# Performance work log

Hardware: AMD Instinct MI355X
Metric: run time of the kernel (lower is better)

Reference implementation:

```python
import jax, jax.numpy as jnp
import numpy as np
from functools import partial

EPS = 1e-5
SCALE = 2
NUM_BLOCKS = 2


def _layernorm(x, g, b):
    mu = jnp.mean(x, axis=-1, keepdims=True)
    var = jnp.var(x, axis=-1, keepdims=True)
    return (x - mu) * jax.lax.rsqrt(var + EPS) * g + b


def _rwkv(tokens, td, Wk, Wv, Wr, Wo, ln_g, ln_b):
    # tokens: (B, N, C)
    x = _layernorm(tokens, ln_g, ln_b)
    k = jnp.einsum('bnc,oc->bno', x, Wk)
    v = jnp.einsum('bnc,oc->bno', x, Wv)
    r = jax.nn.sigmoid(jnp.einsum('bnc,oc->bno', x, Wr))
    decay = jnp.exp(-jax.nn.relu(td))  # (C,)

    def step(state, inp):
        kt, vt, rt = inp  # each (B, C)
        state = state * decay + kt
        return state, rt * (state + vt)

    B, N, C = tokens.shape
    init = jnp.zeros((B, C), dtype=tokens.dtype)
    # scan over token axis
    _, yT = jax.lax.scan(step, init, (k.transpose(1, 0, 2), v.transpose(1, 0, 2), r.transpose(1, 0, 2)))
    y = yT.transpose(1, 0, 2)  # (B, N, C)
    return jnp.einsum('bnc,oc->bno', y, Wo)


def reference(x, global_state, cond_gw, cond_gb, cond_bw, cond_bb,
              td, Wk, Wv, Wr, Wo, ln_g, ln_b, gp_w, gp_b, bp_w, bp_b):
    B, C, H, W = x.shape
    Hp, Wp = H * SCALE, W * SCALE
    # bilinear upsample, half-pixel centers == torch align_corners=False
    x_up = jax.image.resize(x, (B, C, Hp, Wp), method='bilinear')
    tokens = x_up.reshape(B, C, Hp * Wp).transpose(0, 2, 1)  # (B, N, C)
    # semantic conditioning (FiLM from global state)
    gamma = (global_state @ cond_gw.T + cond_gb)[:, None, :]
    beta = (global_state @ cond_bw.T + cond_bb)[:, None, :]
    tokens = tokens * (1.0 + gamma) + beta

    out = x_up
    cur = tokens
    for i in range(NUM_BLOCKS):
        if i > 0:
            cur = out.reshape(B, C, Hp * Wp).transpose(0, 2, 1)
        t = _rwkv(cur, td[i], Wk[i], Wv[i], Wr[i], Wo[i], ln_g[i], ln_b[i])
        g = jnp.einsum('bnc,oc->bno', t, gp_w[i]) + gp_b[i]
        bt = jnp.einsum('bnc,oc->bno', t, bp_w[i]) + bp_b[i]
        g = g.transpose(0, 2, 1).reshape(B, C, Hp, Wp)
        bt = bt.transpose(0, 2, 1).reshape(B, C, Hp, Wp)
        out = out * (1.0 + jnp.tanh(g)) + bt
    return out


def setup_inputs() -> dict:
    key = jax.random.key(0)
    ks = jax.random.split(key, 16)
    B, C, H, W = 8, 128, 64, 64
    w_scale = 0.02
    inp = {
        'x': jax.random.normal(ks[0], (B, C, H, W), jnp.float32),
        'global_state': jax.random.normal(ks[1], (B, C), jnp.float32),
        'cond_gw': jax.random.normal(ks[2], (C, C), jnp.float32) * w_scale,
        'cond_gb': jnp.zeros((C,), jnp.float32),
        'cond_bw': jax.random.normal(ks[3], (C, C), jnp.float32) * w_scale,
        'cond_bb': jnp.zeros((C,), jnp.float32),
        'td': jax.random.uniform(ks[4], (NUM_BLOCKS, C), jnp.float32),
        'Wk': jax.random.normal(ks[5], (NUM_BLOCKS, C, C), jnp.float32) * w_scale,
        'Wv': jax.random.normal(ks[6], (NUM_BLOCKS, C, C), jnp.float32) * w_scale,
        'Wr': jax.random.normal(ks[7], (NUM_BLOCKS, C, C), jnp.float32) * w_scale,
        'Wo': jax.random.normal(ks[8], (NUM_BLOCKS, C, C), jnp.float32) * w_scale,
        'ln_g': jnp.ones((NUM_BLOCKS, C), jnp.float32),
        'ln_b': jnp.zeros((NUM_BLOCKS, C), jnp.float32),
        'gp_w': jax.random.normal(ks[9], (NUM_BLOCKS, C, C), jnp.float32) * w_scale,
        'gp_b': jnp.zeros((NUM_BLOCKS, C), jnp.float32),
        'bp_w': jax.random.normal(ks[10], (NUM_BLOCKS, C, C), jnp.float32) * w_scale,
        'bp_b': jnp.zeros((NUM_BLOCKS, C), jnp.float32),
    }
    return inp
```

## Files before the change

kernel.cpp:

```cpp
#include <hip/hip_runtime.h>
#include <hip/hip_bf16.h>

#define BB 8
#define CC 128
#define NN 16384
#define MM (BB * NN)
#define NCH 128
#define CLN 128

typedef __attribute__((ext_vector_type(8))) short short8;
typedef __attribute__((ext_vector_type(4))) float floatx4;
typedef unsigned short u16;
typedef unsigned int u32;

__device__ __forceinline__ float bf2f(u16 h) {
  u32 u = ((u32)h) << 16;
  return __builtin_bit_cast(float, u);
}
__device__ __forceinline__ u16 f2bf(float f) {
  u32 u = __builtin_bit_cast(u32, f);
  u32 r = u + 0x7FFFu + ((u >> 16) & 1u);
  return (u16)(r >> 16);
}

__global__ void film_kernel(const float* __restrict__ gs, const float* __restrict__ gw,
                            const float* __restrict__ gb, const float* __restrict__ bw,
                            const float* __restrict__ bb, float* __restrict__ gamma,
                            float* __restrict__ beta) {
  int idx = blockIdx.x * 256 + threadIdx.x;
  int b = idx >> 7, c = idx & 127;
  float sg = 0.f, sb = 0.f;
  for (int j = 0; j < 128; ++j) {
    float g = gs[b * 128 + j];
    sg += g * gw[c * 128 + j];
    sb += g * bw[c * 128 + j];
  }
  gamma[idx] = sg + gb[c];
  beta[idx] = sb + bb[c];
}

__global__ void convert_kernel(const float* __restrict__ Wk, const float* __restrict__ Wv,
                               const float* __restrict__ Wr, const float* __restrict__ Wo,
                               const float* __restrict__ gp, const float* __restrict__ bp,
                               u16* __restrict__ dst) {
  int idx = blockIdx.x * 256 + threadIdx.x;
  int which = idx >> 15;
  int off = idx & 32767;
  const float* s;
  switch (which) {
    case 0: s = Wk; break; case 1: s = Wv; break; case 2: s = Wr; break;
    case 3: s = Wo; break; case 4: s = gp; break; default: s = bp; break;
  }
  dst[idx] = f2bf(s[off]);
}

template <int UPS>
__global__ __launch_bounds__(256) void prep_kernel(
    const float* __restrict__ src, const float* __restrict__ gamma,
    const float* __restrict__ beta, const float* __restrict__ lng,
    const float* __restrict__ lnb, float* __restrict__ outp, u16* __restrict__ xn) {
  __shared__ float tile[64][129];
  __shared__ float smu[64], srs[64];
  int bidx = blockIdx.x;
  int half = bidx & 1;
  int ho = (bidx >> 1) & 127;
  int b = bidx >> 8;
  int wo0 = half * 64;
  int tid = threadIdx.x;
  int tk = tid & 63;
  int wo = wo0 + tk;
  int c0 = tid >> 6;
  int j0 = 0, j1 = 0, i0 = 0, i1 = 0;
  float wy0 = 0.f, wy1 = 0.f, wx0 = 0.f, wx1 = 0.f;
  if (UPS) {
    int jj = ho >> 1;
    if ((ho & 1) == 0) { j0 = jj > 0 ? jj - 1 : 0; j1 = jj; wy0 = 0.25f; wy1 = 0.75f; }
    else               { j0 = jj; j1 = jj < 63 ? jj + 1 : 63; wy0 = 0.75f; wy1 = 0.25f; }
    int ii = wo >> 1;
    if ((wo & 1) == 0) { i0 = ii > 0 ? ii - 1 : 0; i1 = ii; wx0 = 0.25f; wx1 = 0.75f; }
    else               { i0 = ii; i1 = ii < 63 ? ii + 1 : 63; wx0 = 0.75f; wx1 = 0.25f; }
  }
  for (int it = 0; it < 32; ++it) {
    int c = it * 4 + c0;
    float v;
    if (UPS) {
      const float* xp = src + ((size_t)(b * 128 + c)) * 4096;
      v = wy0 * (wx0 * xp[j0 * 64 + i0] + wx1 * xp[j0 * 64 + i1]) +
          wy1 * (wx0 * xp[j1 * 64 + i0] + wx1 * xp[j1 * 64 + i1]);
      outp[((size_t)(b * 128 + c)) * 16384 + ho * 128 + wo] = v;
      v = v * (1.f + gamma[b * 128 + c]) + beta[b * 128 + c];
    } else {
      v = src[((size_t)(b * 128 + c)) * 16384 + ho * 128 + wo];
    }
    tile[tk][c] = v;
  }
  __syncthreads();
  {
    int token = tid >> 2, q = tid & 3;
    float s = 0.f, s2 = 0.f;
    for (int j = 0; j < 32; ++j) { float v = tile[token][q * 32 + j]; s += v; s2 += v * v; }
    s += __shfl_xor(s, 1); s2 += __shfl_xor(s2, 1);
    s += __shfl_xor(s, 2); s2 += __shfl_xor(s2, 2);
    if (q == 0) {
      float mu = s * 0.0078125f;
      float var = s2 * 0.0078125f - mu * mu;
      smu[token] = mu;
      srs[token] = rsqrtf(var + 1e-5f);
    }
  }
  __syncthreads();
  size_t base = ((size_t)b * 16384 + ho * 128 + wo0) * 128;
  for (int it = 0; it < 32; ++it) {
    int idx = it * 256 + tid;
    int token = idx >> 7, c = idx & 127;
    float v = (tile[token][c] - smu[token]) * srs[token] * lng[c] + lnb[c];
    xn[base + idx] = f2bf(v);
  }
}

__global__ __launch_bounds__(256) void gemm_kvr_kernel(
    const u16* __restrict__ A, const u16* __restrict__ W0, const u16* __restrict__ W1,
    const u16* __restrict__ W2, const float* __restrict__ td, u16* __restrict__ outK,
    u16* __restrict__ outV, u16* __restrict__ outR, float* __restrict__ Sbuf) {
  __shared__ u16 Alds[128 * 128];
  __shared__ u16 Wlds[128 * 128];
  __shared__ float Sred[512];
  int tid = threadIdx.x;
  int wave = tid >> 6, lane = tid & 63;
  int l15 = lane & 15, l4 = lane >> 4;
  size_t row0 = (size_t)blockIdx.x * 128;
#pragma unroll
  for (int it = 0; it < 8; ++it) {
    int idx = it * 256 + tid;
    int rr = idx >> 4, s = idx & 15;
    uint4 d = *(const uint4*)(A + (row0 + rr) * 128 + s * 8);
    *(uint4*)(&Alds[rr * 128 + ((s ^ (rr & 15)) << 3)]) = d;
  }
  const u16* Wsarr[3] = {W0, W1, W2};
#pragma unroll
  for (int wsi = 0; wsi < 3; ++wsi) {
#pragma unroll
    for (int it = 0; it < 8; ++it) {
      int idx = it * 256 + tid;
      int rr = idx >> 4, s = idx & 15;
      uint4 d = *(const uint4*)(Wsarr[wsi] + rr * 128 + s * 8);
      *(uint4*)(&Wlds[rr * 128 + ((s ^ (rr & 15)) << 3)]) = d;
    }
    __syncthreads();
    floatx4 acc[2][8];
#pragma unroll
    for (int mi = 0; mi < 2; ++mi)
#pragma unroll
      for (int ni = 0; ni < 8; ++ni) acc[mi][ni] = (floatx4){0.f, 0.f, 0.f, 0.f};
#pragma unroll
    for (int kk = 0; kk < 4; ++kk) {
      int seg = kk * 4 + l4;
      short8 a0 = *(const short8*)(&Alds[(wave * 32 + l15) * 128 + ((seg ^ l15) << 3)]);
      short8 a1 = *(const short8*)(&Alds[(wave * 32 + 16 + l15) * 128 + ((seg ^ l15) << 3)]);
#pragma unroll
      for (int ni = 0; ni < 8; ++ni) {
        short8 bfr = *(const short8*)(&Wlds[(ni * 16 + l15) * 128 + ((seg ^ l15) << 3)]);
        acc[0][ni] = __builtin_amdgcn_mfma_f32_16x16x32_bf16(a0, bfr, acc[0][ni], 0, 0, 0);
        acc[1][ni] = __builtin_amdgcn_mfma_f32_16x16x32_bf16(a1, bfr, acc[1][ni], 0, 0, 0);
      }
    }
#pragma unroll
    for (int mi = 0; mi < 2; ++mi) {
#pragma unroll
      for (int ni = 0; ni < 8; ++ni) {
        int col = ni * 16 + l15;
#pragma unroll
        for (int j = 0; j < 4; ++j) {
          size_t row = row0 + wave * 32 + mi * 16 + l4 * 4 + j;
          float val = acc[mi][ni][j];
          if (wsi == 0) outK[row * 128 + col] = f2bf(val);
          else if (wsi == 1) outV[row * 128 + col] = f2bf(val);
          else outR[row * 128 + col] = f2bf(1.f / (1.f + __expf(-val)));
        }
      }
    }
    if (wsi == 0) {
      int T0 = wave * 32 + l4 * 4;
#pragma unroll
      for (int ni = 0; ni < 8; ++ni) {
        int c = ni * 16 + l15;
        float a = fmaxf(td[c], 0.f);
        float E = __expf(-a * (float)(127 - T0));
        float r1 = __expf(a);
        float r2 = r1 * r1, r4 = r2 * r2, r8 = r4 * r4, r16 = r8 * r8;
        float w = E, sum;
        sum  = w * acc[0][ni][0]; w *= r1;
        sum += w * acc[0][ni][1]; w *= r1;
        sum += w * acc[0][ni][2]; w *= r1;
        sum += w * acc[0][ni][3];
        w = E * r16;
        sum += w * acc[1][ni][0]; w *= r1;
        sum += w * acc[1][ni][1]; w *= r1;
        sum += w * acc[1][ni][2]; w *= r1;
        sum += w * acc[1][ni][3];
        sum += __shfl_xor(sum, 16);
        sum += __shfl_xor(sum, 32);
        if (l4 == 0) Sred[wave * 128 + c] = sum;
      }
    }
    __syncthreads();
    if (wsi == 0 && tid < 128) {
      float s = Sred[tid] + Sred[128 + tid] + Sred[256 + tid] + Sred[384 + tid];
      Sbuf[(blockIdx.x & 127) * 1024 + (blockIdx.x >> 7) * 128 + tid] = s;
    }
  }
}

__global__ __launch_bounds__(256) void scan2_kernel(const float* __restrict__ S,
                                                    const float* __restrict__ td,
                                                    float* __restrict__ init) {
  int wave = threadIdx.x >> 6, lane = threadIdx.x & 63;
  int bc = blockIdx.x * 4 + wave;
  int c = bc & 127;
  float a1 = __expf(-fmaxf(td[c], 0.f) * 128.f);
  float s0 = S[(2 * lane) * 1024 + bc];
  float s1 = S[(2 * lane + 1) * 1024 + bc];
  float s = s1 + a1 * s0;
  float a = a1 * a1;
  for (int off = 1; off < 64; off <<= 1) {
    float ss = __shfl_up(s, off);
    float aa = __shfl_up(a, off);
    if (lane >= off) { s = s + a * ss; a = a * aa; }
  }
  float e = __shfl_up(s, 1);
  if (lane == 0) e = 0.f;
  init[(2 * lane) * 1024 + bc] = e;
  init[(2 * lane + 1) * 1024 + bc] = a1 * e + s0;
}

__global__ __launch_bounds__(512, 4) void tail_kernel(
    const u16* __restrict__ k, const u16* __restrict__ v, const u16* __restrict__ r,
    const float* __restrict__ init, const float* __restrict__ td,
    const u16* __restrict__ Wo, const u16* __restrict__ Wg, const u16* __restrict__ Wb,
    const float* __restrict__ gpb, const float* __restrict__ bpb,
    float* __restrict__ outp) {
  __shared__ u32 SMEM[8192];
  __shared__ float SC[512];
  u16* Y = (u16*)SMEM;
  u16* T2 = (u16*)SMEM;
  u32* MB = SMEM;

  int tid = threadIdx.x;
  int wave = tid >> 6, lane = tid & 63;
  int l15 = lane & 15, l4 = lane >> 4;
  int b = blockIdx.x >> 7;
  int chunk = blockIdx.x & 127;
  size_t ebase = ((size_t)b * 16384 + (size_t)chunk * 128) * 128;

  {
    int c = tid & 127;
    int sub = tid >> 7;
    float a = fmaxf(td[c], 0.f);
    float d = __expf(-a);
    const u16* kp = k + ebase + (size_t)sub * 32 * 128 + c;
    const u16* vp = v + ebase + (size_t)sub * 32 * 128 + c;
    const u16* rp = r + ebase + (size_t)sub * 32 * 128 + c;
    float s = 0.f;
#pragma unroll
    for (int t = 0; t < 32; ++t) s = s * d + bf2f(kp[t * 128]);
    SC[sub * 128 + c] = s;
    __syncthreads();
    float st = init[chunk * 1024 + b * 128 + c];
    float d32 = __expf(-a * 32.f);
    for (int j = 0; j < sub; ++j) st = st * d32 + SC[j * 128 + c];
    int cs = c >> 3, cl = c & 7;
#pragma unroll
    for (int t = 0; t < 32; ++t) {
      int tg = sub * 32 + t;
      st = st * d + bf2f(kp[t * 128]);
      float y = bf2f(rp[t * 128]) * (st + bf2f(vp[t * 128]));
      Y[tg * 128 + (((cs ^ (tg & 15)) << 3) | cl)] = f2bf(y);
    }
  }
  __syncthreads();

  int ob = wave * 16;
  short8 wof[4];
#pragma unroll
  for (int kk = 0; kk < 4; ++kk)
    wof[kk] = *(const short8*)(Wo + (ob + l15) * 128 + kk * 32 + l4 * 8);
  floatx4 acc[8];
#pragma unroll
  for (int ni = 0; ni < 8; ++ni) acc[ni] = (floatx4){0.f, 0.f, 0.f, 0.f};
#pragma unroll
  for (int kk = 0; kk < 4; ++kk) {
    int seg = kk * 4 + l4;
#pragma unroll
    for (int ni = 0; ni < 8; ++ni) {
      short8 yf = *(const short8*)(&Y[(ni * 16 + l15) * 128 + ((seg ^ l15) << 3)]);
      acc[ni] = __builtin_amdgcn_mfma_f32_16x16x32_bf16(wof[kk], yf, acc[ni], 0, 0, 0);
    }
  }
  __syncthreads();

#pragma unroll
  for (int ni = 0; ni < 8; ++ni) {
    int tok = ni * 16 + l15;
#pragma unroll
    for (int j = 0; j < 4; j += 2) {
      int o = ob + l4 * 4 + j;
      u32 pack = (u32)f2bf(acc[ni][j]) | ((u32)f2bf(acc[ni][j + 1]) << 16);
      int pos = tok * 128 + ((((o >> 3) ^ (tok & 15)) << 3) | (o & 7));
      *(u32*)(T2 + pos) = pack;
    }
  }
  __syncthreads();

  short8 wgf[4], wbf2[4];
#pragma unroll
  for (int kk = 0; kk < 4; ++kk) {
    wgf[kk]  = *(const short8*)(Wg + (ob + l15) * 128 + kk * 32 + l4 * 8);
    wbf2[kk] = *(const short8*)(Wb + (ob + l15) * 128 + kk * 32 + l4 * 8);
  }
  floatx4 ag[8], ab[8];
#pragma unroll
  for (int ni = 0; ni < 8; ++ni) {
    ag[ni] = (floatx4){0.f, 0.f, 0.f, 0.f};
    ab[ni] = (floatx4){0.f, 0.f, 0.f, 0.f};
  }
#pragma unroll
  for (int kk = 0; kk < 4; ++kk) {
    int seg = kk * 4 + l4;
#pragma unroll
    for (int ni = 0; ni < 8; ++ni) {
      short8 tf = *(const short8*)(&T2[(ni * 16 + l15) * 128 + ((seg ^ l15) << 3)]);
      ag[ni] = __builtin_amdgcn_mfma_f32_16x16x32_bf16(wgf[kk], tf, ag[ni], 0, 0, 0);
      ab[ni] = __builtin_amdgcn_mfma_f32_16x16x32_bf16(wbf2[kk], tf, ab[ni], 0, 0, 0);
    }
  }
  __syncthreads();

#pragma unroll
  for (int h = 0; h < 2; ++h) {
    if ((wave >> 2) == h) {
      int orel0 = (wave & 3) * 16;
#pragma unroll
      for (int ni = 0; ni < 8; ++ni) {
        int tok = ni * 16 + l15;
#pragma unroll
        for (int j = 0; j < 4; ++j) {
          int orel = orel0 + l4 * 4 + j;
          int o = h * 64 + orel;
          float g = ag[ni][j] + gpb[o];
          float t1 = __expf(2.f * g);
          float m = 2.f - 2.f / (t1 + 1.f);
          float bt = ab[ni][j] + bpb[o];
          int rot = ((orel & 3) << 2) | ((orel >> 2) & 3);
          MB[orel * 128 + ((((tok >> 3) ^ rot) << 3) | (tok & 7))] =
              (u32)f2bf(m) | ((u32)f2bf(bt) << 16);
        }
      }
    }
    __syncthreads();
#pragma unroll
    for (int it = 0; it < 2; ++it) {
      int idx = it * 512 + tid;
      int orel = idx >> 4, seg = idx & 15;
      int o = h * 64 + orel;
      int rot = ((orel & 3) << 2) | ((orel >> 2) & 3);
      int sp = ((seg ^ rot) << 3);
      uint4 mb0 = *(const uint4*)(&MB[orel * 128 + sp]);
      uint4 mb1 = *(const uint4*)(&MB[orel * 128 + sp + 4]);
      float* op = outp + ((size_t)(b * 128 + o)) * 16384 + chunk * 128 + seg * 8;
      float4 o0 = *(float4*)op;
      float4 o1 = *(float4*)(op + 4);
      o0.x = o0.x * bf2f((u16)(mb0.x & 0xffff)) + bf2f((u16)(mb0.x >> 16));
      o0.y = o0.y * bf2f((u16)(mb0.y & 0xffff)) + bf2f((u16)(mb0.y >> 16));
      o0.z = o0.z * bf2f((u16)(mb0.z & 0xffff)) + bf2f((u16)(mb0.z >> 16));
      o0.w = o0.w * bf2f((u16)(mb0.w & 0xffff)) + bf2f((u16)(mb0.w >> 16));
      o1.x = o1.x * bf2f((u16)(mb1.x & 0xffff)) + bf2f((u16)(mb1.x >> 16));
      o1.y = o1.y * bf2f((u16)(mb1.y & 0xffff)) + bf2f((u16)(mb1.y >> 16));
      o1.z = o1.z * bf2f((u16)(mb1.z & 0xffff)) + bf2f((u16)(mb1.z >> 16));
      o1.w = o1.w * bf2f((u16)(mb1.w & 0xffff)) + bf2f((u16)(mb1.w >> 16));
      *(float4*)op = o0;
      *(float4*)(op + 4) = o1;
    }
    __syncthreads();
  }
}

extern "C" void kernel_launch(void* const* d_in, const int* in_sizes, int n_in,
                              void* d_out, int out_size, void* d_ws, size_t ws_size,
                              hipStream_t stream) {
  const float* x        = (const float*)d_in[0];
  const float* gs       = (const float*)d_in[1];
  const float* cond_gw  = (const float*)d_in[2];
  const float* cond_gb  = (const float*)d_in[3];
  const float* cond_bw  = (const float*)d_in[4];
  const float* cond_bb  = (const float*)d_in[5];
  const float* td       = (const float*)d_in[6];
  const float* Wk       = (const float*)d_in[7];
  const float* Wv       = (const float*)d_in[8];
  const float* Wr       = (const float*)d_in[9];
  const float* Wo       = (const float*)d_in[10];
  const float* ln_g     = (const float*)d_in[11];
  const float* ln_b     = (const float*)d_in[12];
  const float* gp_w     = (const float*)d_in[13];
  const float* gp_b     = (const float*)d_in[14];
  const float* bp_w     = (const float*)d_in[15];
  const float* bp_b     = (const float*)d_in[16];
  float* outp = (float*)d_out;

  char* w = (char*)d_ws;
  float* gamma = (float*)w; w += 4096;
  float* beta  = (float*)w; w += 4096;
  u16* wbf     = (u16*)w;   w += 6 * 2 * 16384 * sizeof(u16);
  u16* xn      = (u16*)w;   w += (size_t)MM * 128 * sizeof(u16);
  u16* kbuf    = (u16*)w;   w += (size_t)MM * 128 * sizeof(u16);
  u16* vbuf    = (u16*)w;   w += (size_t)MM * 128 * sizeof(u16);
  u16* rbuf    = (u16*)w;   w += (size_t)MM * 128 * sizeof(u16);
  float* Sbuf  = (float*)w; w += NCH * 1024 * sizeof(float);
  float* ibuf  = (float*)w; w += NCH * 1024 * sizeof(float);

  film_kernel<<<4, 256, 0, stream>>>(gs, cond_gw, cond_gb, cond_bw, cond_bb, gamma, beta);
  convert_kernel<<<768, 256, 0, stream>>>(Wk, Wv, Wr, Wo, gp_w, bp_w, wbf);

  for (int blk = 0; blk < 2; ++blk) {
    const u16* bWk = wbf + 0 * 32768 + blk * 16384;
    const u16* bWv = wbf + 1 * 32768 + blk * 16384;
    const u16* bWr = wbf + 2 * 32768 + blk * 16384;
    const u16* bWo = wbf + 3 * 32768 + blk * 16384;
    const u16* bGp = wbf + 4 * 32768 + blk * 16384;
    const u16* bBp = wbf + 5 * 32768 + blk * 16384;
    const float* tdi = td + blk * 128;

    if (blk == 0)
      prep_kernel<1><<<2048, 256, 0, stream>>>(x, gamma, beta, ln_g, ln_b, outp, xn);
    else
      prep_kernel<0><<<2048, 256, 0, stream>>>(outp, nullptr, nullptr, ln_g + 128,
                                               ln_b + 128, nullptr, xn);

    gemm_kvr_kernel<<<1024, 256, 0, stream>>>(xn, bWk, bWv, bWr, tdi,
                                              kbuf, vbuf, rbuf, Sbuf);
    scan2_kernel<<<256, 256, 0, stream>>>(Sbuf, tdi, ibuf);
    tail_kernel<<<1024, 512, 0, stream>>>(kbuf, vbuf, rbuf, ibuf, tdi,
                                          bWo, bGp, bBp, gp_b + blk * 128,
                                          bp_b + blk * 128, outp);
  }
}
```

Before: 265.7 us.

## Fuse intra-chunk scan into KVR GEMM, emit partial y and decayed r

The GEMM kernel now runs the within-chunk linear recurrence in registers, using cross-lane shuffles and shared memory to carry state between waves. It writes a partial output y (computed with zero initial state) and a decay-weighted r, so two bf16 intermediates are stored instead of three k/v/r buffers. The tail kernel then only applies the chunk's incoming state as y + rd*init, with vectorized loads, replacing its serial per-token scan. This reduces global memory traffic and serial work, but adds register pressure (several accumulator sets are live, with launch bounds of 2 blocks) and takes a small precision risk from storing r·decay in bf16.

New measurement: 268.9 us. No clear change (+1.2%).

```diff
diff --git a/kernel.cpp b/kernel.cpp
--- a/kernel.cpp
+++ b/kernel.cpp
@@ -118,17 +118,18 @@
   }
 }
 
-__global__ __launch_bounds__(256) void gemm_kvr_kernel(
-    const u16* __restrict__ A, const u16* __restrict__ W0, const u16* __restrict__ W1,
-    const u16* __restrict__ W2, const float* __restrict__ td, u16* __restrict__ outK,
-    u16* __restrict__ outV, u16* __restrict__ outR, float* __restrict__ Sbuf) {
+__global__ __launch_bounds__(256, 2) void gemm_y_kernel(
+    const u16* __restrict__ A, const u16* __restrict__ Wv_, const u16* __restrict__ Wr_,
+    const u16* __restrict__ Wk_, const float* __restrict__ td,
+    u16* __restrict__ outY, u16* __restrict__ outRD, float* __restrict__ Sbuf) {
   __shared__ u16 Alds[128 * 128];
   __shared__ u16 Wlds[128 * 128];
-  __shared__ float Sred[512];
+  __shared__ float SWT[512];
   int tid = threadIdx.x;
   int wave = tid >> 6, lane = tid & 63;
   int l15 = lane & 15, l4 = lane >> 4;
   size_t row0 = (size_t)blockIdx.x * 128;
+
 #pragma unroll
   for (int it = 0; it < 8; ++it) {
     int idx = it * 256 + tid;
@@ -136,78 +137,192 @@
     uint4 d = *(const uint4*)(A + (row0 + rr) * 128 + s * 8);
     *(uint4*)(&Alds[rr * 128 + ((s ^ (rr & 15)) << 3)]) = d;
   }
-  const u16* Wsarr[3] = {W0, W1, W2};
-#pragma unroll
-  for (int wsi = 0; wsi < 3; ++wsi) {
-#pragma unroll
-    for (int it = 0; it < 8; ++it) {
-      int idx = it * 256 + tid;
-      int rr = idx >> 4, s = idx & 15;
-      uint4 d = *(const uint4*)(Wsarr[wsi] + rr * 128 + s * 8);
-      *(uint4*)(&Wlds[rr * 128 + ((s ^ (rr & 15)) << 3)]) = d;
-    }
-    __syncthreads();
-    floatx4 acc[2][8];
-#pragma unroll
-    for (int mi = 0; mi < 2; ++mi)
-#pragma unroll
-      for (int ni = 0; ni < 8; ++ni) acc[mi][ni] = (floatx4){0.f, 0.f, 0.f, 0.f};
-#pragma unroll
-    for (int kk = 0; kk < 4; ++kk) {
-      int seg = kk * 4 + l4;
-      short8 a0 = *(const short8*)(&Alds[(wave * 32 + l15) * 128 + ((seg ^ l15) << 3)]);
-      short8 a1 = *(const short8*)(&Alds[(wave * 32 + 16 + l15) * 128 + ((seg ^ l15) << 3)]);
-#pragma unroll
-      for (int ni = 0; ni < 8; ++ni) {
-        short8 bfr = *(const short8*)(&Wlds[(ni * 16 + l15) * 128 + ((seg ^ l15) << 3)]);
-        acc[0][ni] = __builtin_amdgcn_mfma_f32_16x16x32_bf16(a0, bfr, acc[0][ni], 0, 0, 0);
-        acc[1][ni] = __builtin_amdgcn_mfma_f32_16x16x32_bf16(a1, bfr, acc[1][ni], 0, 0, 0);
+#pragma unroll
+  for (int it = 0; it < 8; ++it) {
+    int idx = it * 256 + tid;
+    int rr = idx >> 4, s = idx & 15;
+    uint4 d = *(const uint4*)(Wv_ + rr * 128 + s * 8);
+    *(uint4*)(&Wlds[rr * 128 + ((s ^ (rr & 15)) << 3)]) = d;
+  }
+  float av[8], dd[8], d4a[8];
+#pragma unroll
+  for (int ni = 0; ni < 8; ++ni) {
+    float a = fmaxf(td[ni * 16 + l15], 0.f);
+    av[ni] = a;
+    float d = __expf(-a);
+    dd[ni] = d;
+    float d2 = d * d;
+    d4a[ni] = d2 * d2;
+  }
+  __syncthreads();
+
+  floatx4 accv[2][8];
+#pragma unroll
+  for (int mi = 0; mi < 2; ++mi)
+#pragma unroll
+    for (int ni = 0; ni < 8; ++ni) accv[mi][ni] = (floatx4){0.f, 0.f, 0.f, 0.f};
+#pragma unroll
+  for (int kk = 0; kk < 4; ++kk) {
+    int seg = kk * 4 + l4;
+    short8 a0 = *(const short8*)(&Alds[(wave * 32 + l15) * 128 + ((seg ^ l15) << 3)]);
+    short8 a1 = *(const short8*)(&Alds[(wave * 32 + 16 + l15) * 128 + ((seg ^ l15) << 3)]);
+#pragma unroll
+    for (int ni = 0; ni < 8; ++ni) {
+      short8 bfr = *(const short8*)(&Wlds[(ni * 16 + l15) * 128 + ((seg ^ l15) << 3)]);
+      accv[0][ni] = __builtin_amdgcn_mfma_f32_16x16x32_bf16(a0, bfr, accv[0][ni], 0, 0, 0);
+      accv[1][ni] = __builtin_amdgcn_mfma_f32_16x16x32_bf16(a1, bfr, accv[1][ni], 0, 0, 0);
+    }
+  }
+  __syncthreads();
+#pragma unroll
+  for (int it = 0; it < 8; ++it) {
+    int idx = it * 256 + tid;
+    int rr = idx >> 4, s = idx & 15;
+    uint4 d = *(const uint4*)(Wr_ + rr * 128 + s * 8);
+    *(uint4*)(&Wlds[rr * 128 + ((s ^ (rr & 15)) << 3)]) = d;
+  }
+  __syncthreads();
+  floatx4 accr[2][8];
+#pragma unroll
+  for (int mi = 0; mi < 2; ++mi)
+#pragma unroll
+    for (int ni = 0; ni < 8; ++ni) accr[mi][ni] = (floatx4){0.f, 0.f, 0.f, 0.f};
+#pragma unroll
+  for (int kk = 0; kk < 4; ++kk) {
+    int seg = kk * 4 + l4;
+    short8 a0 = *(const short8*)(&Alds[(wave * 32 + l15) * 128 + ((seg ^ l15) << 3)]);
+    short8 a1 = *(const short8*)(&Alds[(wave * 32 + 16 + l15) * 128 + ((seg ^ l15) << 3)]);
+#pragma unroll
+    for (int ni = 0; ni < 8; ++ni) {
+      short8 bfr = *(const short8*)(&Wlds[(ni * 16 + l15) * 128 + ((seg ^ l15) << 3)]);
+      accr[0][ni] = __builtin_amdgcn_mfma_f32_16x16x32_bf16(a0, bfr, accr[0][ni], 0, 0, 0);
+      accr[1][ni] = __builtin_amdgcn_mfma_f32_16x16x32_bf16(a1, bfr, accr[1][ni], 0, 0, 0);
+    }
+  }
+  u32 rvp[2][8][2], rp[2][8][2];
+#pragma unroll
+  for (int mi = 0; mi < 2; ++mi) {
+#pragma unroll
+    for (int ni = 0; ni < 8; ++ni) {
+      int c = ni * 16 + l15;
+      int T0 = wave * 32 + mi * 16 + l4 * 4;
+      float w = __expf(-av[ni] * (float)(T0 + 1));
+      float rs[4], rv[4];
+#pragma unroll
+      for (int j = 0; j < 4; ++j) {
+        float sg = 1.f / (1.f + __expf(-accr[mi][ni][j]));
+        rs[j] = sg;
+        rv[j] = sg * accv[mi][ni][j];
+        outRD[(row0 + T0 + j) * 128 + c] = f2bf(sg * w);
+        w *= dd[ni];
       }
-    }
+      rvp[mi][ni][0] = (u32)f2bf(rv[0]) | ((u32)f2bf(rv[1]) << 16);
+      rvp[mi][ni][1] = (u32)f2bf(rv[2]) | ((u32)f2bf(rv[3]) << 16);
+      rp[mi][ni][0] = (u32)f2bf(rs[0]) | ((u32)f2bf(rs[1]) << 16);
+      rp[mi][ni][1] = (u32)f2bf(rs[2]) | ((u32)f2bf(rs[3]) << 16);
+    }
+  }
+  __syncthreads();
+#pragma unroll
+  for (int it = 0; it < 8; ++it) {
+    int idx = it * 256 + tid;
+    int rr = idx >> 4, s = idx & 15;
+    uint4 d = *(const uint4*)(Wk_ + rr * 128 + s * 8);
+    *(uint4*)(&Wlds[rr * 128 + ((s ^ (rr & 15)) << 3)]) = d;
+  }
+  __syncthreads();
+  floatx4 acck[2][8];
+#pragma unroll
+  for (int mi = 0; mi < 2; ++mi)
+#pragma unroll
+    for (int ni = 0; ni < 8; ++ni) acck[mi][ni] = (floatx4){0.f, 0.f, 0.f, 0.f};
+#pragma unroll
+  for (int kk = 0; kk < 4; ++kk) {
+    int seg = kk * 4 + l4;
+    short8 a0 = *(const short8*)(&Alds[(wave * 32 + l15) * 128 + ((seg ^ l15) << 3)]);
+    short8 a1 = *(const short8*)(&Alds[(wave * 32 + 16 + l15) * 128 + ((seg ^ l15) << 3)]);
+#pragma unroll
+    for (int ni = 0; ni < 8; ++ni) {
+      short8 bfr = *(const short8*)(&Wlds[(ni * 16 + l15) * 128 + ((seg ^ l15) << 3)]);
+      acck[0][ni] = __builtin_amdgcn_mfma_f32_16x16x32_bf16(a0, bfr, acck[0][ni], 0, 0, 0);
+      acck[1][ni] = __builtin_amdgcn_mfma_f32_16x16x32_bf16(a1, bfr, acck[1][ni], 0, 0, 0);
+    }
+  }
+  float Elr[2][8];
+  float B0r[8];
+#pragma unroll
+  for (int ni = 0; ni < 8; ++ni) {
+    float d = dd[ni], d4 = d4a[ni];
+    float d8 = d4 * d4, d16 = d8 * d8;
+    float I[2];
 #pragma unroll
     for (int mi = 0; mi < 2; ++mi) {
-#pragma unroll
-      for (int ni = 0; ni < 8; ++ni) {
-        int col = ni * 16 + l15;
-#pragma unroll
-        for (int j = 0; j < 4; ++j) {
-          size_t row = row0 + wave * 32 + mi * 16 + l4 * 4 + j;
-          float val = acc[mi][ni][j];
-          if (wsi == 0) outK[row * 128 + col] = f2bf(val);
-          else if (wsi == 1) outV[row * 128 + col] = f2bf(val);
-          else outR[row * 128 + col] = f2bf(1.f / (1.f + __expf(-val)));
-        }
+      float p0 = acck[mi][ni][0];
+      float p1 = d * p0 + acck[mi][ni][1];
+      float p2 = d * p1 + acck[mi][ni][2];
+      float p3 = d * p2 + acck[mi][ni][3];
+      acck[mi][ni][0] = p0; acck[mi][ni][1] = p1;
+      acck[mi][ni][2] = p2; acck[mi][ni][3] = p3;
+      float Iv = p3;
+      float t1 = __shfl_up(Iv, 16);
+      if (l4 >= 1) Iv += d4 * t1;
+      float t2 = __shfl_up(Iv, 32);
+      if (l4 >= 2) Iv += d8 * t2;
+      float ex = __shfl_up(Iv, 16);
+      Elr[mi][ni] = (l4 == 0) ? 0.f : ex;
+      I[mi] = Iv;
+    }
+    float B0 = __shfl(I[0], 48 + l15);
+    float B1 = __shfl(I[1], 48 + l15);
+    B0r[ni] = B0;
+    if (l4 == 0) SWT[wave * 128 + ni * 16 + l15] = B1 + d16 * B0;
+  }
+  __syncthreads();
+  u16* YW = Wlds;
+#pragma unroll
+  for (int ni = 0; ni < 8; ++ni) {
+    int c = ni * 16 + l15;
+    float d = dd[ni], d4 = d4a[ni];
+    float d8 = d4 * d4, d12 = d8 * d4, d16 = d8 * d8, d32 = d16 * d16;
+    float e = 0.f;
+#pragma unroll
+    for (int wv = 0; wv < 3; ++wv)
+      if (wv < wave) e = e * d32 + SWT[wv * 128 + c];
+    float d4l = (l4 == 0) ? 1.f : ((l4 == 1) ? d4 : ((l4 == 2) ? d8 : d12));
+#pragma unroll
+    for (int mi = 0; mi < 2; ++mi) {
+      float Emi = (mi == 0) ? e : (e * d16 + B0r[ni]);
+      float Sb = Elr[mi][ni] + d4l * Emi;
+      float w = d;
+#pragma unroll
+      for (int j = 0; j < 4; ++j) {
+        float s = acck[mi][ni][j] + w * Sb;
+        w *= d;
+        float rvv = bf2f((u16)(rvp[mi][ni][j >> 1] >> ((j & 1) * 16)));
+        float rss = bf2f((u16)(rp[mi][ni][j >> 1] >> ((j & 1) * 16)));
+        float y = rvv + rss * s;
+        int row = wave * 32 + mi * 16 + l4 * 4 + j;
+        int colsw = c ^ (((row >> 2) & 3) << 4);
+        YW[row * 128 + colsw] = f2bf(y);
       }
     }
-    if (wsi == 0) {
-      int T0 = wave * 32 + l4 * 4;
-#pragma unroll
-      for (int ni = 0; ni < 8; ++ni) {
-        int c = ni * 16 + l15;
-        float a = fmaxf(td[c], 0.f);
-        float E = __expf(-a * (float)(127 - T0));
-        float r1 = __expf(a);
-        float r2 = r1 * r1, r4 = r2 * r2, r8 = r4 * r4, r16 = r8 * r8;
-        float w = E, sum;
-        sum  = w * acc[0][ni][0]; w *= r1;
-        sum += w * acc[0][ni][1]; w *= r1;
-        sum += w * acc[0][ni][2]; w *= r1;
-        sum += w * acc[0][ni][3];
-        w = E * r16;
-        sum += w * acc[1][ni][0]; w *= r1;
-        sum += w * acc[1][ni][1]; w *= r1;
-        sum += w * acc[1][ni][2]; w *= r1;
-        sum += w * acc[1][ni][3];
-        sum += __shfl_xor(sum, 16);
-        sum += __shfl_xor(sum, 32);
-        if (l4 == 0) Sred[wave * 128 + c] = sum;
-      }
-    }
-    __syncthreads();
-    if (wsi == 0 && tid < 128) {
-      float s = Sred[tid] + Sred[128 + tid] + Sred[256 + tid] + Sred[384 + tid];
-      Sbuf[(blockIdx.x & 127) * 1024 + (blockIdx.x >> 7) * 128 + tid] = s;
-    }
+  }
+  if (tid < 128) {
+    float a = fmaxf(td[tid], 0.f);
+    float d32 = __expf(-32.f * a);
+    float e = 0.f;
+#pragma unroll
+    for (int wv = 0; wv < 4; ++wv) e = e * d32 + SWT[wv * 128 + tid];
+    Sbuf[(blockIdx.x & 127) * 1024 + (blockIdx.x >> 7) * 128 + tid] = e;
+  }
+  __syncthreads();
+#pragma unroll
+  for (int it = 0; it < 8; ++it) {
+    int idx = it * 256 + tid;
+    int row = idx >> 4, cb = (idx & 15) * 8;
+    int csw = cb ^ (((row >> 2) & 3) << 4);
+    uint4 dv = *(const uint4*)(&YW[row * 128 + csw]);
+    *(uint4*)(outY + (row0 + row) * 128 + cb) = dv;
   }
 }
 
@@ -234,13 +349,13 @@
 }
 
 __global__ __launch_bounds__(512, 4) void tail_kernel(
-    const u16* __restrict__ k, const u16* __restrict__ v, const u16* __restrict__ r,
-    const float* __restrict__ init, const float* __restrict__ td,
+    const u16* __restrict__ yl, const u16* __restrict__ rd,
+    const float* __restrict__ init,
     const u16* __restrict__ Wo, const u16* __restrict__ Wg, const u16* __restrict__ Wb,
     const float* __restrict__ gpb, const float* __restrict__ bpb,
     float* __restrict__ outp) {
   __shared__ u32 SMEM[8192];
-  __shared__ float SC[512];
+  __shared__ float IL[128];
   u16* Y = (u16*)SMEM;
   u16* T2 = (u16*)SMEM;
   u32* MB = SMEM;
@@ -252,30 +367,27 @@
   int chunk = blockIdx.x & 127;
   size_t ebase = ((size_t)b * 16384 + (size_t)chunk * 128) * 128;
 
-  {
-    int c = tid & 127;
-    int sub = tid >> 7;
-    float a = fmaxf(td[c], 0.f);
-    float d = __expf(-a);
-    const u16* kp = k + ebase + (size_t)sub * 32 * 128 + c;
-    const u16* vp = v + ebase + (size_t)sub * 32 * 128 + c;
-    const u16* rp = r + ebase + (size_t)sub * 32 * 128 + c;
-    float s = 0.f;
-#pragma unroll
-    for (int t = 0; t < 32; ++t) s = s * d + bf2f(kp[t * 128]);
-    SC[sub * 128 + c] = s;
-    __syncthreads();
-    float st = init[chunk * 1024 + b * 128 + c];
-    float d32 = __expf(-a * 32.f);
-    for (int j = 0; j < sub; ++j) st = st * d32 + SC[j * 128 + c];
-    int cs = c >> 3, cl = c & 7;
-#pragma unroll
-    for (int t = 0; t < 32; ++t) {
-      int tg = sub * 32 + t;
-      st = st * d + bf2f(kp[t * 128]);
-      float y = bf2f(rp[t * 128]) * (st + bf2f(vp[t * 128]));
-      Y[tg * 128 + (((cs ^ (tg & 15)) << 3) | cl)] = f2bf(y);
-    }
+  if (tid < 128) IL[tid] = init[chunk * 1024 + b * 128 + tid];
+  __syncthreads();
+
+#pragma unroll
+  for (int it = 0; it < 4; ++it) {
+    int idx = it * 512 + tid;
+    int t = idx >> 4;
+    int c8 = (idx & 15) * 8;
+    uint4 yv = *(const uint4*)(yl + ebase + (size_t)t * 128 + c8);
+    uint4 rv = *(const uint4*)(rd + ebase + (size_t)t * 128 + c8);
+    u32 o[4];
+    u32 yq[4] = {yv.x, yv.y, yv.z, yv.w};
+    u32 rq[4] = {rv.x, rv.y, rv.z, rv.w};
+#pragma unroll
+    for (int q = 0; q < 4; ++q) {
+      float y0 = bf2f((u16)(yq[q] & 0xffff)) + bf2f((u16)(rq[q] & 0xffff)) * IL[c8 + 2 * q];
+      float y1 = bf2f((u16)(yq[q] >> 16)) + bf2f((u16)(rq[q] >> 16)) * IL[c8 + 2 * q + 1];
+      o[q] = (u32)f2bf(y0) | ((u32)f2bf(y1) << 16);
+    }
+    uint4 ov = {o[0], o[1], o[2], o[3]};
+    *(uint4*)(&Y[t * 128 + (((c8 >> 3) ^ (t & 15)) << 3)]) = ov;
   }
   __syncthreads();
 
@@ -411,9 +523,8 @@
   float* beta  = (float*)w; w += 4096;
   u16* wbf     = (u16*)w;   w += 6 * 2 * 16384 * sizeof(u16);
   u16* xn      = (u16*)w;   w += (size_t)MM * 128 * sizeof(u16);
-  u16* kbuf    = (u16*)w;   w += (size_t)MM * 128 * sizeof(u16);
-  u16* vbuf    = (u16*)w;   w += (size_t)MM * 128 * sizeof(u16);
-  u16* rbuf    = (u16*)w;   w += (size_t)MM * 128 * sizeof(u16);
+  u16* ybuf    = (u16*)w;   w += (size_t)MM * 128 * sizeof(u16);
+  u16* rdbuf   = (u16*)w;   w += (size_t)MM * 128 * sizeof(u16);
   float* Sbuf  = (float*)w; w += NCH * 1024 * sizeof(float);
   float* ibuf  = (float*)w; w += NCH * 1024 * sizeof(float);
 
@@ -435,11 +546,9 @@
       prep_kernel<0><<<2048, 256, 0, stream>>>(outp, nullptr, nullptr, ln_g + 128,
                                                ln_b + 128, nullptr, xn);
 
-    gemm_kvr_kernel<<<1024, 256, 0, stream>>>(xn, bWk, bWv, bWr, tdi,
-                                              kbuf, vbuf, rbuf, Sbuf);
+    gemm_y_kernel<<<1024, 256, 0, stream>>>(xn, bWv, bWr, bWk, tdi, ybuf, rdbuf, Sbuf);
     scan2_kernel<<<256, 256, 0, stream>>>(Sbuf, tdi, ibuf);
-    tail_kernel<<<1024, 512, 0, stream>>>(kbuf, vbuf, rbuf, ibuf, tdi,
-                                          bWo, bGp, bBp, gp_b + blk * 128,
-                                          bp_b + blk * 128, outp);
-  }
-}
+    tail_kernel<<<1024, 512, 0, stream>>>(ybuf, rdbuf, ibuf, bWo, bGp, bBp,
+                                          gp_b + blk * 128, bp_b + blk * 128, outp);
+  }
+}
```
